# Kernel tuning notes

Hardware: AMD Instinct MI355X
Metric: run time of the kernel (lower is better)

Reference implementation:

```python
import jax, jax.numpy as jnp
import numpy as np

B, N, F_IN, F_OUT, H = 4, 2048, 256, 256, 4
NEG_INF = -1e9
EDGE_PROB = 0.05
LEAKY_SLOPE = 0.2  # tf.nn.leaky_relu default alpha


def setup_inputs() -> dict:
    key = jax.random.key(0)
    k_x, k_m, k_w, k_a, k_b = jax.random.split(key, 5)
    inputs = jax.random.normal(k_x, (B, N, F_IN), dtype=jnp.float32)
    # bias: additive adjacency mask, 0 on edges / -1e9 off-edges (standard GAT)
    u = jax.random.uniform(k_m, (B, N, N), dtype=jnp.float32)
    bias = jnp.where(u < EDGE_PROB, 0.0, NEG_INF).astype(jnp.float32)
    # self-loops so every softmax row has at least one valid entry
    bias = bias.at[:, jnp.arange(N), jnp.arange(N)].set(0.0)
    # per-head learned params (uniform [0,1) init as in the original)
    W = jax.random.uniform(k_w, (H, F_IN, F_OUT), dtype=jnp.float32)
    a = jax.random.uniform(k_a, (H, F_OUT), dtype=jnp.float32)
    b = jax.random.uniform(k_b, (H, F_OUT), dtype=jnp.float32)
    return {"inputs": inputs, "bias": bias, "W": W, "a": a, "b": b}


def reference(inputs, bias, W, a, b):
    # transformed: [H, B, N, F_OUT]
    t = jnp.einsum('bnf,hfo->hbno', inputs, W) + b[:, None, None, :]
    # per-node score s = t @ a : [H, B, N]
    s = jnp.einsum('hbno,ho->hbn', t, a)
    # weights[i,j] = s[i] + s[j]  (weights + transpose)
    w = s[..., :, None] + s[..., None, :]  # [H, B, N, N]
    coefs = jax.nn.softmax(jax.nn.leaky_relu(w, negative_slope=LEAKY_SLOPE) + bias, axis=-1)
    heads = jnp.einsum('hbnm,hbmo->hbno', coefs, t)  # [H, B, N, F_OUT]
    return jnp.mean(heads, axis=0)  # (1/num_heads) * add_n(heads)
```

## Files before the change

kernel.cpp:

```cpp
#include <hip/hip_runtime.h>
#include <hip/hip_bf16.h>
#include <stdint.h>

#define H 4
#define BB 4
#define NN 2048
#define FIN 256
#define FOUT 256
#define M_TOT (BB*NN)
#define LOG2E 1.44269504f

typedef float f32x4 __attribute__((ext_vector_type(4)));
typedef short s16x8 __attribute__((ext_vector_type(8)));
typedef unsigned int u32;

static __device__ __forceinline__ short f2bf(float f) {
    return __builtin_bit_cast(short, __float2bfloat16(f));
}
static __device__ __forceinline__ float bf2f(short u) {
    unsigned x = ((unsigned)(unsigned short)u) << 16;
    return __builtin_bit_cast(float, x);
}

__global__ __launch_bounds__(256) void k_prep(const float* __restrict__ W, const float* __restrict__ a,
                                              const float* __restrict__ bvec,
                                              short* __restrict__ WT, float* __restrict__ q,
                                              float* __restrict__ c) {
    int bid = blockIdx.x;
    if (bid < 64) {
        __shared__ float lds[64][65];
        int h = bid >> 4, kt = (bid >> 2) & 3, ot = bid & 3;
        int kb = kt * 64, ob = ot * 64;
        int tx = threadIdx.x & 63, ty = threadIdx.x >> 6;
#pragma unroll
        for (int r = 0; r < 16; ++r) {
            int k_l = ty + r * 4;
            lds[tx][k_l] = W[(size_t)(h * FIN + kb + k_l) * FOUT + ob + tx];
        }
        __syncthreads();
#pragma unroll
        for (int r = 0; r < 16; ++r) {
            int o_l = ty + r * 4;
            WT[(size_t)(h * FOUT + ob + o_l) * FIN + kb + tx] = f2bf(lds[o_l][tx]);
        }
    } else if (bid < 320) {
        int wv = ((bid - 64) * 256 + threadIdx.x) >> 6;
        int lane = threadIdx.x & 63;
        int h = wv >> 8, f = wv & 255;
        float4 w4 = *(const float4*)(W + (size_t)(h * FIN + f) * FOUT + lane * 4);
        float4 a4 = *(const float4*)(a + h * FOUT + lane * 4);
        float d = w4.x * a4.x + w4.y * a4.y + w4.z * a4.z + w4.w * a4.w;
#pragma unroll
        for (int off = 32; off; off >>= 1) d += __shfl_xor(d, off);
        if (lane == 0) q[h * FIN + f] = d;
    } else {
        int h = threadIdx.x >> 6, lane = threadIdx.x & 63;
        float4 b4 = *(const float4*)(bvec + h * FOUT + lane * 4);
        float4 a4 = *(const float4*)(a + h * FOUT + lane * 4);
        float d = b4.x * a4.x + b4.y * a4.y + b4.z * a4.z + b4.w * a4.w;
#pragma unroll
        for (int off = 32; off; off >>= 1) d += __shfl_xor(d, off);
        if (lane == 0) c[h] = d;
    }
}

__global__ __launch_bounds__(256) void k_s(const float* __restrict__ X, const float* __restrict__ q,
                                           const float* __restrict__ c, float* __restrict__ s,
                                           short* __restrict__ Xbf) {
    int m = blockIdx.x * 4 + (threadIdx.x >> 6);
    int lane = threadIdx.x & 63;
    float4 xv = *(const float4*)(X + (size_t)m * FIN + lane * 4);
    short4 xb;
    xb.x = f2bf(xv.x); xb.y = f2bf(xv.y); xb.z = f2bf(xv.z); xb.w = f2bf(xv.w);
    *(short4*)(Xbf + (size_t)m * FIN + lane * 4) = xb;
#pragma unroll
    for (int h = 0; h < H; ++h) {
        float4 qv = *(const float4*)(q + h * FIN + lane * 4);
        float d = xv.x * qv.x + xv.y * qv.y + xv.z * qv.z + xv.w * qv.w;
#pragma unroll
        for (int off = 32; off; off >>= 1) d += __shfl_xor(d, off);
        if (lane == 0) s[h * M_TOT + m] = d + c[h];
    }
}

__global__ __launch_bounds__(256) void k_maskmax(const float* __restrict__ bias, const float* __restrict__ s,
                                                 unsigned* __restrict__ mask, float* __restrict__ mx) {
    __shared__ float sl[8192];
    int tid = threadIdx.x;
    int row0 = blockIdx.x * 4;
    int b = row0 >> 11;
#pragma unroll
    for (int i = 0; i < 8; ++i) {
        int flat = i * 1024 + tid * 4;
        int h = flat >> 11, j = flat & 2047;
        float4 v = *(const float4*)(s + (size_t)h * M_TOT + (size_t)b * NN + j);
        int phys = flat ^ (((flat >> 5) & 7) << 2);
        *(float4*)(sl + phys) = v;
    }
    __syncthreads();

    int w = tid >> 6, lane = tid & 63;
    int row = row0 + w;
    const float* bp = bias + (size_t)row * NN + lane * 32;
    unsigned bits = 0;
#pragma unroll
    for (int k = 0; k < 8; ++k) {
        float4 v = *(const float4*)(bp + k * 4);
        bits |= (v.x > -1.f ? 1u : 0u) << (k * 4 + 0);
        bits |= (v.y > -1.f ? 1u : 0u) << (k * 4 + 1);
        bits |= (v.z > -1.f ? 1u : 0u) << (k * 4 + 2);
        bits |= (v.w > -1.f ? 1u : 0u) << (k * 4 + 3);
    }
    mask[(size_t)row * 64 + lane] = bits;
#pragma unroll
    for (int h = 0; h < H; ++h) {
        float m = -3e38f;
#pragma unroll
        for (int k = 0; k < 8; ++k) {
            int flat = h * 2048 + lane * 32 + k * 4;
            int phys = flat ^ (((flat >> 5) & 7) << 2);
            float4 sv = *(const float4*)(sl + phys);
            m = fmaxf(m, ((bits >> (k * 4 + 0)) & 1u) ? sv.x : -3e38f);
            m = fmaxf(m, ((bits >> (k * 4 + 1)) & 1u) ? sv.y : -3e38f);
            m = fmaxf(m, ((bits >> (k * 4 + 2)) & 1u) ? sv.z : -3e38f);
            m = fmaxf(m, ((bits >> (k * 4 + 3)) & 1u) ? sv.w : -3e38f);
        }
#pragma unroll
        for (int off = 32; off; off >>= 1) m = fmaxf(m, __shfl_xor(m, off));
        if (lane == 0) mx[h * M_TOT + row] = m;
    }
}

__global__ __launch_bounds__(256) void k_gemm_t(const short* __restrict__ WT, const short* __restrict__ Xbf,
                                                const float* __restrict__ bvec, short* __restrict__ tTs) {
    __shared__ short ot[64][136];
    int h = blockIdx.z;
    int ob = blockIdx.y * 64;
    int mb = blockIdx.x * 128;
    int tid = threadIdx.x;
    int lane = tid & 63, w = tid >> 6;
    int r16 = lane & 15, g = lane >> 4;
    int mw = mb + w * 32;
    f32x4 acc[4][2] = {};
    for (int k = 0; k < FIN; k += 32) {
        s16x8 afr[4], bfr[2];
#pragma unroll
        for (int fa = 0; fa < 4; ++fa)
            afr[fa] = *(const s16x8*)(WT + (size_t)(h * FOUT + ob + fa * 16 + r16) * FIN + k + g * 8);
#pragma unroll
        for (int fb = 0; fb < 2; ++fb)
            bfr[fb] = *(const s16x8*)(Xbf + (size_t)(mw + fb * 16 + r16) * FIN + k + g * 8);
#pragma unroll
        for (int fa = 0; fa < 4; ++fa)
#pragma unroll
            for (int fb = 0; fb < 2; ++fb)
                acc[fa][fb] = __builtin_amdgcn_mfma_f32_16x16x32_bf16(afr[fa], bfr[fb], acc[fa][fb], 0, 0, 0);
    }
#pragma unroll
    for (int fa = 0; fa < 4; ++fa) {
#pragma unroll
        for (int r = 0; r < 4; ++r) {
            int o_l = fa * 16 + g * 4 + r;
            float bv = bvec[h * FOUT + ob + o_l];
#pragma unroll
            for (int fb = 0; fb < 2; ++fb)
                ot[o_l][w * 32 + fb * 16 + r16] = f2bf(acc[fa][fb][r] + bv);
        }
    }
    __syncthreads();
    int bb = mb >> 11, jloc = mb & 2047;
    int jt0 = jloc >> 6;
    size_t slab = (size_t)((h * 4 + bb) * 32) * 16384;
#pragma unroll
    for (int cc = 0; cc < 4; ++cc) {
        int sid = cc * 256 + tid;
        int frag = sid >> 6;
        int l = sid & 63;
        int f_l = frag >> 2, jt_sel = (frag >> 1) & 1, par = frag & 1;
        int o_l = f_l * 16 + (l & 15);
        int m_l = jt_sel * 64 + par * 32 + (l >> 4) * 8;
        s16x8 v = *(const s16x8*)&ot[o_l][m_l];
        int fid = ((ob >> 4) + f_l) * 2 + par;
        size_t addr = slab + (size_t)(jt0 + jt_sel) * 16384 + fid * 512 + l * 8;
        *(s16x8*)(tTs + addr) = v;
    }
}

__global__ __launch_bounds__(512, 4) void k_attn(const short* __restrict__ tTs, const float* __restrict__ s,
                                                 const unsigned* __restrict__ mask, const float* __restrict__ mx,
                                                 short* __restrict__ OT) {
    __shared__ short smem[16640];

    int flat = blockIdx.x + 32 * (blockIdx.y + 4 * blockIdx.z);
    int swz = (flat & 7) * 64 + (flat >> 3);
    int qt = swz & 31, b = (swz >> 5) & 3, h = swz >> 7;
    int ib = qt * 64;

    int tid = threadIdx.x;
    int lane = tid & 63, w = tid >> 6;
    int r16 = lane & 15, g = lane >> 4;
    int par = w & 1, oh = w >> 1;
    size_t gm = (size_t)b * NN;

    const short* slab = tTs + (size_t)((h * 4 + b) * 32) * 16384;
    const float* srow = s + h * M_TOT + gm;

    int i = ib + oh * 16 + r16;
    float si = srow[i];
    float mxi = mx[h * M_TOT + gm + i];
    float z = si + mxi;
    float Mlog = fmaxf(z, 0.2f * z) * LOG2E;
    float siL = si * LOG2E;
    const unsigned* mk = mask + (gm + i) * 64;

    int chk = ((((par << 2) + g) ^ (r16 & 7)) << 3);
    int rdP = r16 * 64 + chk;
    int wrP = oh * 1024 + rdP;

    f32x4 acc[4][4] = {};
    float lsum = 0.f;

    s16x8 acur[4], anext[4];
#pragma unroll
    for (int f = 0; f < 4; ++f)
        acur[f] = *(const s16x8*)(slab + ((oh * 4 + f) * 2 + par) * 512 + lane * 8);

    float4 psj0, psj1; unsigned pwm;
    {
        int jw = par * 32;
        psj0 = *(const float4*)(srow + jw + g * 8);
        psj1 = *(const float4*)(srow + jw + g * 8 + 4);
        pwm = mk[par];
    }

    for (int t = 0; t < 32; ++t) {
        if (t < 31) {
            const short* tp = slab + (size_t)(t + 1) * 16384;
#pragma unroll
            for (int f = 0; f < 4; ++f)
                anext[f] = *(const s16x8*)(tp + ((oh * 4 + f) * 2 + par) * 512 + lane * 8);
        }

        float sjv[8] = {psj0.x, psj0.y, psj0.z, psj0.w, psj1.x, psj1.y, psj1.z, psj1.w};
        unsigned bb0 = pwm >> (g * 8);
        s16x8 pb;
#pragma unroll
        for (int e = 0; e < 8; ++e) {
            float yL = fmaf(sjv[e], LOG2E, siL);
            float ly = fmaxf(yL, 0.2f * yL);
            float aa = ((bb0 >> e) & 1u) ? (ly - Mlog) : -200.f;
            short pv = f2bf(__builtin_amdgcn_exp2f(aa));
            pb[e] = pv;
            lsum += bf2f(pv);
        }
        *(s16x8*)(smem + (t & 1) * 4096 + wrP) = pb;

        if (t < 31) {
            int jw = (t + 1) * 64 + par * 32;
            psj0 = *(const float4*)(srow + jw + g * 8);
            psj1 = *(const float4*)(srow + jw + g * 8 + 4);
            pwm = mk[(t + 1) * 2 + par];
        }

        asm volatile("s_waitcnt lgkmcnt(0)" ::: "memory");
        __builtin_amdgcn_sched_barrier(0);
        __builtin_amdgcn_s_barrier();
        __builtin_amdgcn_sched_barrier(0);

        const short* Pb = smem + (t & 1) * 4096;
        __builtin_amdgcn_s_setprio(1);
#pragma unroll
        for (int qf = 0; qf < 4; ++qf) {
            s16x8 pf = *(const s16x8*)(Pb + qf * 1024 + rdP);
            acc[0][qf] = __builtin_amdgcn_mfma_f32_16x16x32_bf16(acur[0], pf, acc[0][qf], 0, 0, 0);
            acc[1][qf] = __builtin_amdgcn_mfma_f32_16x16x32_bf16(acur[1], pf, acc[1][qf], 0, 0, 0);
            acc[2][qf] = __builtin_amdgcn_mfma_f32_16x16x32_bf16(acur[2], pf, acc[2][qf], 0, 0, 0);
            acc[3][qf] = __builtin_amdgcn_mfma_f32_16x16x32_bf16(acur[3], pf, acc[3][qf], 0, 0, 0);
        }
        __builtin_amdgcn_s_setprio(0);

        if (t < 31) {
#pragma unroll
            for (int f = 0; f < 4; ++f) acur[f] = anext[f];
        }
    }

    __syncthreads();
    lsum += __shfl_xor(lsum, 16);
    lsum += __shfl_xor(lsum, 32);
    float* pl    = (float*)(smem + 16384);
    float* plinv = pl + 64;
    if (par == 1 && g == 0) pl[oh * 16 + r16] = lsum;
    __syncthreads();
    if (par == 0 && g == 0) plinv[oh * 16 + r16] = 1.f / (lsum + pl[oh * 16 + r16]);
    __syncthreads();
    float linv[4];
#pragma unroll
    for (int qf = 0; qf < 4; ++qf) linv[qf] = plinv[qf * 16 + r16];

    f32x4* ex = (f32x4*)smem;
    size_t hbase = (size_t)h * FOUT * M_TOT + gm;
#pragma unroll
    for (int rnd = 0; rnd < 2; ++rnd) {
        if (par == 1 && (oh >> 1) == rnd) {
#pragma unroll
            for (int f = 0; f < 4; ++f)
#pragma unroll
                for (int qf = 0; qf < 4; ++qf)
                    ex[(((oh & 1) * 4 + f) * 4 + qf) * 64 + lane] = acc[f][qf];
        }
        __syncthreads();
        if (par == 0 && (oh >> 1) == rnd) {
#pragma unroll
            for (int f = 0; f < 4; ++f)
#pragma unroll
                for (int qf = 0; qf < 4; ++qf) {
                    f32x4 v = acc[f][qf] + ex[(((oh & 1) * 4 + f) * 4 + qf) * 64 + lane];
                    int iq = ib + qf * 16 + r16;
#pragma unroll
                    for (int rr = 0; rr < 4; ++rr) {
                        int o = (oh * 4 + f) * 16 + g * 4 + rr;
                        OT[hbase + (size_t)o * M_TOT + iq] = f2bf(v[rr] * linv[qf]);
                    }
                }
        }
        __syncthreads();
    }
}

__global__ __launch_bounds__(256) void k_reduce(const short* __restrict__ OT, float* __restrict__ out) {
    __shared__ float lds[32][72];
    int mb = blockIdx.x * 64, obt = blockIdx.y * 32;
    int tid = threadIdx.x;
    {
        int o_l = tid >> 3;
        int m_l = (tid & 7) * 8;
        float acc[8] = {};
#pragma unroll
        for (int h = 0; h < H; ++h) {
            s16x8 v = *(const s16x8*)(OT + (size_t)(h * FOUT + obt + o_l) * M_TOT + mb + m_l);
#pragma unroll
            for (int e = 0; e < 8; ++e) acc[e] += bf2f(v[e]);
        }
#pragma unroll
        for (int e = 0; e < 8; ++e) lds[o_l][m_l + e] = acc[e] * 0.25f;
    }
    __syncthreads();
    {
        int m_l = tid >> 2;
        int o_l = (tid & 3) * 8;
        float4 v0, v1;
        v0.x = lds[o_l + 0][m_l]; v0.y = lds[o_l + 1][m_l];
        v0.z = lds[o_l + 2][m_l]; v0.w = lds[o_l + 3][m_l];
        v1.x = lds[o_l + 4][m_l]; v1.y = lds[o_l + 5][m_l];
        v1.z = lds[o_l + 6][m_l]; v1.w = lds[o_l + 7][m_l];
        float* dst = out + (size_t)(mb + m_l) * FOUT + obt + o_l;
        *(float4*)dst = v0;
        *(float4*)(dst + 4) = v1;
    }
}

extern "C" void kernel_launch(void* const* d_in, const int* in_sizes, int n_in,
                              void* d_out, int out_size, void* d_ws, size_t ws_size,
                              hipStream_t stream) {
    const float* X    = (const float*)d_in[0];
    const float* bias = (const float*)d_in[1];
    const float* W    = (const float*)d_in[2];
    const float* a    = (const float*)d_in[3];
    const float* bvec = (const float*)d_in[4];
    float* out = (float*)d_out;

    char* ws = (char*)d_ws;
    short*    Xbf  = (short*)ws;
    short*    WT   = (short*)(ws + (4u << 20));
    float*    q    = (float*)(ws + (4u << 20) + (768u << 10));
    float*    c    = q + H * FIN;
    float*    s    = (float*)(ws + (5u << 20));
    float*    mxp  = (float*)(ws + (5u << 20) + (256u << 10));
    short*    tTs  = (short*)(ws + (6u << 20));
    short*    OT   = (short*)(ws + (22u << 20));
    unsigned* mask = (unsigned*)(ws + (38u << 20));

    k_prep<<<321, 256, 0, stream>>>(W, a, bvec, WT, q, c);
    k_s<<<2048, 256, 0, stream>>>(X, q, c, s, Xbf);
    k_maskmax<<<2048, 256, 0, stream>>>(bias, s, mask, mxp);
    k_gemm_t<<<dim3(64, 4, 4), 256, 0, stream>>>(WT, Xbf, bvec, tTs);
    k_attn<<<dim3(32, 4, 4), 512, 0, stream>>>(tTs, s, mask, mxp, OT);
    k_reduce<<<dim3(128, 8), 256, 0, stream>>>(OT, out);
}
```

Measured before the change: 114.9 us.

## Stage attention output in LDS for row-major writes and simplify head reduction

```diff
diff --git a/kernel.cpp b/kernel.cpp
--- a/kernel.cpp
+++ b/kernel.cpp
@@ -188,8 +188,8 @@
 
 __global__ __launch_bounds__(512, 4) void k_attn(const short* __restrict__ tTs, const float* __restrict__ s,
                                                  const unsigned* __restrict__ mask, const float* __restrict__ mx,
-                                                 short* __restrict__ OT) {
-    __shared__ short smem[16640];
+                                                 short* __restrict__ OTn) {
+    __shared__ short smem[34048];
 
     int flat = blockIdx.x + 32 * (blockIdx.y + 4 * blockIdx.z);
     int swz = (flat & 7) * 64 + (flat >> 3);
@@ -211,6 +211,9 @@
     float z = si + mxi;
     float Mlog = fmaxf(z, 0.2f * z) * LOG2E;
     float siL = si * LOG2E;
+    float c1 = siL - Mlog;
+    float c2 = 0.2f * siL - Mlog;
+    const float k1 = LOG2E, k2 = 0.2f * LOG2E;
     const unsigned* mk = mask + (gm + i) * 64;
 
     int chk = ((((par << 2) + g) ^ (r16 & 7)) << 3);
@@ -246,12 +249,13 @@
         s16x8 pb;
 #pragma unroll
         for (int e = 0; e < 8; ++e) {
-            float yL = fmaf(sjv[e], LOG2E, siL);
-            float ly = fmaxf(yL, 0.2f * yL);
-            float aa = ((bb0 >> e) & 1u) ? (ly - Mlog) : -200.f;
-            short pv = f2bf(__builtin_amdgcn_exp2f(aa));
-            pb[e] = pv;
-            lsum += bf2f(pv);
+            float u = fmaf(sjv[e], k1, c1);
+            float vv = fmaf(sjv[e], k2, c2);
+            float aa = fmaxf(u, vv);
+            aa = ((bb0 >> e) & 1u) ? aa : -200.f;
+            float p = __builtin_amdgcn_exp2f(aa);
+            lsum += p;
+            pb[e] = f2bf(p);
         }
         *(s16x8*)(smem + (t & 1) * 4096 + wrP) = pb;
 
@@ -288,7 +292,7 @@
     __syncthreads();
     lsum += __shfl_xor(lsum, 16);
     lsum += __shfl_xor(lsum, 32);
-    float* pl    = (float*)(smem + 16384);
+    float* pl    = (float*)((char*)smem + 67584);
     float* plinv = pl + 64;
     if (par == 1 && g == 0) pl[oh * 16 + r16] = lsum;
     __syncthreads();
@@ -298,16 +302,19 @@
 #pragma unroll
     for (int qf = 0; qf < 4; ++qf) linv[qf] = plinv[qf * 16 + r16];
 
-    f32x4* ex = (f32x4*)smem;
-    size_t hbase = (size_t)h * FOUT * M_TOT + gm;
+    float* exf  = (float*)smem;
+    short* outT = smem + 16896;
 #pragma unroll
     for (int rnd = 0; rnd < 2; ++rnd) {
         if (par == 1 && (oh >> 1) == rnd) {
 #pragma unroll
             for (int f = 0; f < 4; ++f)
 #pragma unroll
-                for (int qf = 0; qf < 4; ++qf)
-                    ex[(((oh & 1) * 4 + f) * 4 + qf) * 64 + lane] = acc[f][qf];
+                for (int qf = 0; qf < 4; ++qf) {
+                    int irow = qf * 16 + r16;
+                    int o_loc = (oh & 1) * 64 + f * 16 + g * 4;
+                    *(f32x4*)(exf + irow * 132 + o_loc) = acc[f][qf];
+                }
         }
         __syncthreads();
         if (par == 0 && (oh >> 1) == rnd) {
@@ -315,49 +322,42 @@
             for (int f = 0; f < 4; ++f)
 #pragma unroll
                 for (int qf = 0; qf < 4; ++qf) {
-                    f32x4 v = acc[f][qf] + ex[(((oh & 1) * 4 + f) * 4 + qf) * 64 + lane];
-                    int iq = ib + qf * 16 + r16;
-#pragma unroll
-                    for (int rr = 0; rr < 4; ++rr) {
-                        int o = (oh * 4 + f) * 16 + g * 4 + rr;
-                        OT[hbase + (size_t)o * M_TOT + iq] = f2bf(v[rr] * linv[qf]);
-                    }
+                    int irow = qf * 16 + r16;
+                    int o_loc = (oh & 1) * 64 + f * 16 + g * 4;
+                    f32x4 v = acc[f][qf] + *(const f32x4*)(exf + irow * 132 + o_loc);
+                    short4 o4;
+                    o4.x = f2bf(v[0] * linv[qf]); o4.y = f2bf(v[1] * linv[qf]);
+                    o4.z = f2bf(v[2] * linv[qf]); o4.w = f2bf(v[3] * linv[qf]);
+                    *(short4*)(outT + irow * 264 + rnd * 128 + o_loc) = o4;
                 }
         }
         __syncthreads();
     }
-}
-
-__global__ __launch_bounds__(256) void k_reduce(const short* __restrict__ OT, float* __restrict__ out) {
-    __shared__ float lds[32][72];
-    int mb = blockIdx.x * 64, obt = blockIdx.y * 32;
-    int tid = threadIdx.x;
+
     {
-        int o_l = tid >> 3;
-        int m_l = (tid & 7) * 8;
-        float acc[8] = {};
-#pragma unroll
-        for (int h = 0; h < H; ++h) {
-            s16x8 v = *(const s16x8*)(OT + (size_t)(h * FOUT + obt + o_l) * M_TOT + mb + m_l);
-#pragma unroll
-            for (int e = 0; e < 8; ++e) acc[e] += bf2f(v[e]);
-        }
-#pragma unroll
-        for (int e = 0; e < 8; ++e) lds[o_l][m_l + e] = acc[e] * 0.25f;
-    }
-    __syncthreads();
-    {
-        int m_l = tid >> 2;
-        int o_l = (tid & 3) * 8;
-        float4 v0, v1;
-        v0.x = lds[o_l + 0][m_l]; v0.y = lds[o_l + 1][m_l];
-        v0.z = lds[o_l + 2][m_l]; v0.w = lds[o_l + 3][m_l];
-        v1.x = lds[o_l + 4][m_l]; v1.y = lds[o_l + 5][m_l];
-        v1.z = lds[o_l + 6][m_l]; v1.w = lds[o_l + 7][m_l];
-        float* dst = out + (size_t)(mb + m_l) * FOUT + obt + o_l;
-        *(float4*)dst = v0;
-        *(float4*)(dst + 4) = v1;
-    }
+        int row = tid >> 3, col = (tid & 7) * 32;
+        const short* src = outT + row * 264 + col;
+        size_t gdst = ((size_t)h * M_TOT + gm + ib + row) * 256 + col;
+#pragma unroll
+        for (int cc = 0; cc < 4; ++cc)
+            *(s16x8*)(OTn + gdst + cc * 8) = *(const s16x8*)(src + cc * 8);
+    }
+}
+
+__global__ __launch_bounds__(256) void k_reduce(const short* __restrict__ OTn, float* __restrict__ out) {
+    size_t idx = ((size_t)blockIdx.x * 256 + threadIdx.x) * 8;
+    float acc[8] = {};
+#pragma unroll
+    for (int h = 0; h < H; ++h) {
+        s16x8 v = *(const s16x8*)(OTn + (size_t)h * M_TOT * 256 + idx);
+#pragma unroll
+        for (int e = 0; e < 8; ++e) acc[e] += bf2f(v[e]);
+    }
+    float4 o0, o1;
+    o0.x = acc[0] * 0.25f; o0.y = acc[1] * 0.25f; o0.z = acc[2] * 0.25f; o0.w = acc[3] * 0.25f;
+    o1.x = acc[4] * 0.25f; o1.y = acc[5] * 0.25f; o1.z = acc[6] * 0.25f; o1.w = acc[7] * 0.25f;
+    *(float4*)(out + idx) = o0;
+    *(float4*)(out + idx + 4) = o1;
 }
 
 extern "C" void kernel_launch(void* const* d_in, const int* in_sizes, int n_in,
@@ -378,13 +378,13 @@
     float*    s    = (float*)(ws + (5u << 20));
     float*    mxp  = (float*)(ws + (5u << 20) + (256u << 10));
     short*    tTs  = (short*)(ws + (6u << 20));
-    short*    OT   = (short*)(ws + (22u << 20));
+    short*    OTn  = (short*)(ws + (22u << 20));
     unsigned* mask = (unsigned*)(ws + (38u << 20));
 
     k_prep<<<321, 256, 0, stream>>>(W, a, bvec, WT, q, c);
     k_s<<<2048, 256, 0, stream>>>(X, q, c, s, Xbf);
     k_maskmax<<<2048, 256, 0, stream>>>(bias, s, mask, mxp);
     k_gemm_t<<<dim3(64, 4, 4), 256, 0, stream>>>(WT, Xbf, bvec, tTs);
-    k_attn<<<dim3(32, 4, 4), 512, 0, stream>>>(tTs, s, mask, mxp, OT);
-    k_reduce<<<dim3(128, 8), 256, 0, stream>>>(OT, out);
-}
+    k_attn<<<dim3(32, 4, 4), 512, 0, stream>>>(tTs, s, mask, mxp, OTn);
+    k_reduce<<<1024, 256, 0, stream>>>(OTn, out);
+}
```

Measured after the change: 117.3 us. 1.02x slower.

## Precompute softmax log-sum-exp in mask kernel, drop normalization from attention

Applied to the files above, without the earlier changes.

```diff
diff --git a/kernel.cpp b/kernel.cpp
--- a/kernel.cpp
+++ b/kernel.cpp
@@ -84,7 +84,7 @@
 }
 
 __global__ __launch_bounds__(256) void k_maskmax(const float* __restrict__ bias, const float* __restrict__ s,
-                                                 unsigned* __restrict__ mask, float* __restrict__ mx) {
+                                                 unsigned* __restrict__ mask, float* __restrict__ mtot) {
     __shared__ float sl[8192];
     int tid = threadIdx.x;
     int row0 = blockIdx.x * 4;
@@ -101,6 +101,7 @@
 
     int w = tid >> 6, lane = tid & 63;
     int row = row0 + w;
+    int iloc = row & 2047;
     const float* bp = bias + (size_t)row * NN + lane * 32;
     unsigned bits = 0;
 #pragma unroll
@@ -127,7 +128,30 @@
         }
 #pragma unroll
         for (int off = 32; off; off >>= 1) m = fmaxf(m, __shfl_xor(m, off));
-        if (lane == 0) mx[h * M_TOT + row] = m;
+        int sidx = h * 2048 + iloc;
+        float si = sl[sidx ^ (((sidx >> 5) & 7) << 2)];
+        float z = si + m;
+        float Mlog = fmaxf(z, 0.2f * z) * LOG2E;
+        float c1 = si * LOG2E - Mlog;
+        float c2 = 0.2f * si * LOG2E - Mlog;
+        const float k1 = LOG2E, k2 = 0.2f * LOG2E;
+        float l = 0.f;
+#pragma unroll
+        for (int k = 0; k < 8; ++k) {
+            int flat = h * 2048 + lane * 32 + k * 4;
+            int phys = flat ^ (((flat >> 5) & 7) << 2);
+            float4 sv = *(const float4*)(sl + phys);
+            float svv[4] = {sv.x, sv.y, sv.z, sv.w};
+#pragma unroll
+            for (int e = 0; e < 4; ++e) {
+                float aa = fmaxf(fmaf(svv[e], k1, c1), fmaf(svv[e], k2, c2));
+                aa = ((bits >> (k * 4 + e)) & 1u) ? aa : -200.f;
+                l += __builtin_amdgcn_exp2f(aa);
+            }
+        }
+#pragma unroll
+        for (int off = 32; off; off >>= 1) l += __shfl_xor(l, off);
+        if (lane == 0) mtot[h * M_TOT + row] = Mlog + __builtin_amdgcn_logf(l);
     }
 }
 
@@ -187,7 +211,7 @@
 }
 
 __global__ __launch_bounds__(512, 4) void k_attn(const short* __restrict__ tTs, const float* __restrict__ s,
-                                                 const unsigned* __restrict__ mask, const float* __restrict__ mx,
+                                                 const unsigned* __restrict__ mask, const float* __restrict__ mtot,
                                                  short* __restrict__ OT) {
     __shared__ short smem[16640];
 
@@ -207,10 +231,10 @@
 
     int i = ib + oh * 16 + r16;
     float si = srow[i];
-    float mxi = mx[h * M_TOT + gm + i];
-    float z = si + mxi;
-    float Mlog = fmaxf(z, 0.2f * z) * LOG2E;
-    float siL = si * LOG2E;
+    float mt = mtot[h * M_TOT + gm + i];
+    float c1 = si * LOG2E - mt;
+    float c2 = 0.2f * si * LOG2E - mt;
+    const float k1 = LOG2E, k2 = 0.2f * LOG2E;
     const unsigned* mk = mask + (gm + i) * 64;
 
     int chk = ((((par << 2) + g) ^ (r16 & 7)) << 3);
@@ -218,7 +242,6 @@
     int wrP = oh * 1024 + rdP;
 
     f32x4 acc[4][4] = {};
-    float lsum = 0.f;
 
     s16x8 acur[4], anext[4];
 #pragma unroll
@@ -246,12 +269,11 @@
         s16x8 pb;
 #pragma unroll
         for (int e = 0; e < 8; ++e) {
-            float yL = fmaf(sjv[e], LOG2E, siL);
-            float ly = fmaxf(yL, 0.2f * yL);
-            float aa = ((bb0 >> e) & 1u) ? (ly - Mlog) : -200.f;
-            short pv = f2bf(__builtin_amdgcn_exp2f(aa));
-            pb[e] = pv;
-            lsum += bf2f(pv);
+            float u = fmaf(sjv[e], k1, c1);
+            float vv = fmaf(sjv[e], k2, c2);
+            float aa = fmaxf(u, vv);
+            aa = ((bb0 >> e) & 1u) ? aa : -200.f;
+            pb[e] = f2bf(__builtin_amdgcn_exp2f(aa));
         }
         *(s16x8*)(smem + (t & 1) * 4096 + wrP) = pb;
 
@@ -286,18 +308,6 @@
     }
 
     __syncthreads();
-    lsum += __shfl_xor(lsum, 16);
-    lsum += __shfl_xor(lsum, 32);
-    float* pl    = (float*)(smem + 16384);
-    float* plinv = pl + 64;
-    if (par == 1 && g == 0) pl[oh * 16 + r16] = lsum;
-    __syncthreads();
-    if (par == 0 && g == 0) plinv[oh * 16 + r16] = 1.f / (lsum + pl[oh * 16 + r16]);
-    __syncthreads();
-    float linv[4];
-#pragma unroll
-    for (int qf = 0; qf < 4; ++qf) linv[qf] = plinv[qf * 16 + r16];
-
     f32x4* ex = (f32x4*)smem;
     size_t hbase = (size_t)h * FOUT * M_TOT + gm;
 #pragma unroll
@@ -320,7 +330,7 @@
 #pragma unroll
                     for (int rr = 0; rr < 4; ++rr) {
                         int o = (oh * 4 + f) * 16 + g * 4 + rr;
-                        OT[hbase + (size_t)o * M_TOT + iq] = f2bf(v[rr] * linv[qf]);
+                        OT[hbase + (size_t)o * M_TOT + iq] = f2bf(v[rr]);
                     }
                 }
         }
@@ -376,15 +386,15 @@
     float*    q    = (float*)(ws + (4u << 20) + (768u << 10));
     float*    c    = q + H * FIN;
     float*    s    = (float*)(ws + (5u << 20));
-    float*    mxp  = (float*)(ws + (5u << 20) + (256u << 10));
+    float*    mtot = (float*)(ws + (5u << 20) + (256u << 10));
     short*    tTs  = (short*)(ws + (6u << 20));
     short*    OT   = (short*)(ws + (22u << 20));
     unsigned* mask = (unsigned*)(ws + (38u << 20));
 
     k_prep<<<321, 256, 0, stream>>>(W, a, bvec, WT, q, c);
     k_s<<<2048, 256, 0, stream>>>(X, q, c, s, Xbf);
-    k_maskmax<<<2048, 256, 0, stream>>>(bias, s, mask, mxp);
+    k_maskmax<<<2048, 256, 0, stream>>>(bias, s, mask, mtot);
     k_gemm_t<<<dim3(64, 4, 4), 256, 0, stream>>>(WT, Xbf, bvec, tTs);
-    k_attn<<<dim3(32, 4, 4), 512, 0, stream>>>(tTs, s, mask, mxp, OT);
+    k_attn<<<dim3(32, 4, 4), 512, 0, stream>>>(tTs, s, mask, mtot, OT);
     k_reduce<<<dim3(128, 8), 256, 0, stream>>>(OT, out);
 }
```

Result: slower. 120.7 us (+5.1%).
